# Optimization experiments

Measured on AMD Instinct MI355X. Metric: run time of the kernel, lower is better.

Reference implementation:

```python
import jax, jax.numpy as jnp
import numpy as np

N_HEADS = 8
WINDOW = 4
KS = 3
N_LAYERS = 6
EPS = 1e-5


def _rel_to_abs(x):
    # x: [B,H,L,2L-1] relative logits -> [B,H,L,L] absolute
    b, h, l, _ = x.shape
    x = jnp.pad(x, ((0, 0), (0, 0), (0, 0), (0, 1)))
    x = x.reshape(b, h, l * 2 * l)
    x = jnp.pad(x, ((0, 0), (0, 0), (0, l - 1)))
    return x.reshape(b, h, l + 1, 2 * l - 1)[:, :, :l, l - 1:]


def _abs_to_rel(x):
    # x: [B,H,L,L] -> [B,H,L,2L-1]
    b, h, l, _ = x.shape
    x = jnp.pad(x, ((0, 0), (0, 0), (0, 0), (0, l - 1)))
    x = x.reshape(b, h, l * (2 * l - 1))
    x = jnp.pad(x, ((0, 0), (0, 0), (l, 0)))
    return x.reshape(b, h, l, 2 * l)[:, :, :, 1:]


def _get_rel_emb(emb, t):
    # emb: [2*WINDOW+1, D] -> [2t-1, D]
    pad = max(t - (WINDOW + 1), 0)
    start = max((WINDOW + 1) - t, 0)
    emb = jnp.pad(emb, ((pad, pad), (0, 0)))
    return emb[start:start + 2 * t - 1]


def _layer_norm(x, g, b):
    # normalize over channel dim (axis 1) of [B,C,T]
    m = jnp.mean(x, axis=1, keepdims=True)
    v = jnp.mean((x - m) ** 2, axis=1, keepdims=True)
    return (x - m) * jax.lax.rsqrt(v + EPS) * g[None, :, None] + b[None, :, None]


def _attn(x, w, bvec, erk, erv, attn_mask):
    # x: [B,C,T]; w: [4,C,C] (q,k,v,o 1x1 convs); bvec: [4,C]
    B, C, T = x.shape
    kch = C // N_HEADS

    def proj(i):
        h = jnp.einsum('oc,bct->bot', w[i], x) + bvec[i][None, :, None]
        return h.reshape(B, N_HEADS, kch, T).transpose(0, 1, 3, 2)  # [B,H,T,D]

    q, k, v = proj(0), proj(1), proj(2)
    scale = np.float32(1.0 / np.sqrt(kch))
    scores = jnp.einsum('bhtd,bhsd->bhts', q * scale, k)
    kr = _get_rel_emb(erk, T)  # [2T-1, D]
    scores = scores + _rel_to_abs(jnp.einsum('bhtd,md->bhtm', q * scale, kr))
    scores = jnp.where(attn_mask == 0, jnp.float32(-1e4), scores)
    p = jax.nn.softmax(scores, axis=-1)
    out = jnp.einsum('bhts,bhsd->bhtd', p, v)
    vr = _get_rel_emb(erv, T)
    out = out + jnp.einsum('bhtm,md->bhtd', _abs_to_rel(p), vr)
    out = out.transpose(0, 1, 3, 2).reshape(B, C, T)
    return jnp.einsum('oc,bct->bot', w[3], out) + bvec[3][None, :, None]


def _conv1d_same(h, wt, bt):
    pad_l, pad_r = (KS - 1) // 2, KS // 2
    hp = jnp.pad(h, ((0, 0), (0, 0), (pad_l, pad_r)))
    y = jax.lax.conv_general_dilated(hp, wt, (1,), 'VALID',
                                     dimension_numbers=('NCH', 'OIH', 'NCH'))
    return y + bt[None, :, None]


def _ffn(x, mask, w1, b1, w2, b2):
    h = jax.nn.relu(_conv1d_same(x * mask, w1, b1))  # activation=None -> relu
    return _conv1d_same(h * mask, w2, b2) * mask


def reference(x, x_mask, attn_w, attn_b, erk, erv, ln1_g, ln1_b,
              ffn_w1, ffn_b1, ffn_w2, ffn_b2, ln2_g, ln2_b):
    attn_mask = x_mask[:, :, :, None] * x_mask[:, :, None, :]  # [B,1,T,T]
    x = x * x_mask
    for i in range(N_LAYERS):
        y = _attn(x, attn_w[i], attn_b[i], erk[i], erv[i], attn_mask)
        x = _layer_norm(x + y, ln1_g[i], ln1_b[i])
        y = _ffn(x, x_mask, ffn_w1[i], ffn_b1[i], ffn_w2[i], ffn_b2[i])
        x = _layer_norm(x + y, ln2_g[i], ln2_b[i])
    return x * x_mask


def setup_inputs() -> dict:
    B, C, T, F, L = 8, 512, 1024, 2048, N_LAYERS
    kch = C // N_HEADS
    key = jax.random.key(0)
    ks = jax.random.split(key, 8)
    std = 0.02
    return {
        'x': jax.random.normal(ks[0], (B, C, T), jnp.float32),
        'x_mask': jnp.ones((B, 1, T), jnp.float32),
        'attn_w': jax.random.normal(ks[1], (L, 4, C, C), jnp.float32) * std,
        'attn_b': jnp.zeros((L, 4, C), jnp.float32),
        'erk': jax.random.normal(ks[2], (L, 2 * WINDOW + 1, kch), jnp.float32) * (kch ** -0.5),
        'erv': jax.random.normal(ks[3], (L, 2 * WINDOW + 1, kch), jnp.float32) * (kch ** -0.5),
        'ln1_g': jnp.ones((L, C), jnp.float32),
        'ln1_b': jnp.zeros((L, C), jnp.float32),
        'ffn_w1': jax.random.normal(ks[4], (L, F, C, KS), jnp.float32) * std,
        'ffn_b1': jnp.zeros((L, F), jnp.float32),
        'ffn_w2': jax.random.normal(ks[5], (L, C, F, KS), jnp.float32) * std,
        'ffn_b2': jnp.zeros((L, C), jnp.float32),
        'ln2_g': jnp.ones((L, C), jnp.float32),
        'ln2_b': jnp.zeros((L, C), jnp.float32),
    }
```

## Files before the change

kernel.cpp:

```cpp
#include <hip/hip_runtime.h>

typedef __bf16 bf16_t;
typedef __bf16 bf16x8 __attribute__((ext_vector_type(8)));
typedef __bf16 bf16x4 __attribute__((ext_vector_type(4)));
typedef float  f32x4  __attribute__((ext_vector_type(4)));

#define AS1 __attribute__((address_space(1)))
#define AS3 __attribute__((address_space(3)))

template<int BM, int BN, int OUTMN, int CONV, int BIAS, int RELU, int MASK>
__global__ __launch_bounds__(256)
void gemm_nt(const bf16_t* __restrict__ A, const bf16_t* __restrict__ B,
             bf16_t* __restrict__ C, const float* __restrict__ bias,
             const float* __restrict__ mask, const bf16_t* __restrict__ zpage,
             int K, int lda, int ldb, int ldc, int CIN,
             long sAb, long sAh, long sBb, long sBh, long sCb, long sCh)
{
    constexpr int BK = 32;
    __shared__ bf16_t As[BM * BK];
    __shared__ bf16_t Bs[BN * BK];
    const int z = blockIdx.z;
    int tap0 = 0;
    if constexpr (CONV == 2) {
        tap0 = z;
        A += (long)tap0 * CIN;
    } else {
        A += (long)(z >> 3) * sAb + (long)(z & 7) * sAh;
        B += (long)(z >> 3) * sBb + (long)(z & 7) * sBh;
        C += (long)(z >> 3) * sCb + (long)(z & 7) * sCh;
    }
    const int m0 = blockIdx.y * BM;
    const int n0 = blockIdx.x * BN;
    const int tid = threadIdx.x;
    const int wid = tid >> 6, lane = tid & 63;
    constexpr int WM = BM / 2, WN = BN / 2;
    constexpr int FM = WM / 16, FN = WN / 16;
    const int wm = wid >> 1, wn = wid & 1;

    f32x4 acc[FM][FN] = {};

    constexpr int ACH = BM / 64;
    constexpr int BCH = BN / 64;
    const int rquad = lane >> 2;
    const int koff  = (lane & 3) * 8;

    int tap = 0, cc0 = 0;
    for (int k0 = 0; k0 < K; k0 += BK) {
        #pragma unroll
        for (int q = 0; q < ACH; ++q) {
            int ch  = wid * ACH + q;
            int row = ch * 16 + rquad;
            const bf16_t* src = A + (long)(m0 + row) * lda + (k0 + koff);
            __builtin_amdgcn_global_load_lds((const AS1 void*)src,
                                             (AS3 void*)(As + ch * 512), 16, 0, 0);
        }
        #pragma unroll
        for (int q = 0; q < BCH; ++q) {
            int ch  = wid * BCH + q;
            int row = ch * 16 + rquad;
            const bf16_t* src;
            if constexpr (CONV == 1) {
                int tl = (n0 & 1023) + row + tap - 1;
                src = ((unsigned)tl < 1024u)
                    ? B + (long)(n0 + row + tap - 1) * ldb + (cc0 + koff)
                    : zpage + koff;
            } else if constexpr (CONV == 2) {
                int tl = (n0 & 1023) + row + tap0 - 1;
                src = ((unsigned)tl < 1024u)
                    ? B + (long)(n0 + row + tap0 - 1) * ldb + (k0 + koff)
                    : zpage + koff;
            } else {
                src = B + (long)(n0 + row) * ldb + (k0 + koff);
            }
            __builtin_amdgcn_global_load_lds((const AS1 void*)src,
                                             (AS3 void*)(Bs + ch * 512), 16, 0, 0);
        }
        if constexpr (CONV == 1) { cc0 += BK; if (cc0 == CIN) { cc0 = 0; ++tap; } }
        __syncthreads();

        const bf16_t* Ab = As + (wm * WM + (lane & 15)) * BK + ((lane >> 4) * 8);
        const bf16_t* Bb = Bs + (wn * WN + (lane & 15)) * BK + ((lane >> 4) * 8);
        bf16x8 af[FM], bv[FN];
        #pragma unroll
        for (int i = 0; i < FM; ++i) af[i] = *(const bf16x8*)(Ab + i * 16 * BK);
        #pragma unroll
        for (int j = 0; j < FN; ++j) bv[j] = *(const bf16x8*)(Bb + j * 16 * BK);
        #pragma unroll
        for (int i = 0; i < FM; ++i)
            #pragma unroll
            for (int j = 0; j < FN; ++j)
                acc[i][j] = __builtin_amdgcn_mfma_f32_16x16x32_bf16(af[i], bv[j], acc[i][j], 0, 0, 0);
        __syncthreads();
    }

    const int mw = m0 + wm * WM, nw = n0 + wn * WN;
    #pragma unroll
    for (int i = 0; i < FM; ++i) {
        const int mb = mw + i * 16 + (lane >> 4) * 4;
        f32x4 bvv = {};
        if constexpr (BIAS) bvv = *(const f32x4*)(bias + mb);
        #pragma unroll
        for (int j = 0; j < FN; ++j) {
            const int nn = nw + j * 16 + (lane & 15);
            f32x4 v = acc[i][j];
            if constexpr (BIAS) v += bvv;
            if constexpr (RELU) {
                #pragma unroll
                for (int r = 0; r < 4; ++r) v[r] = fmaxf(v[r], 0.f);
            }
            if constexpr (MASK) v *= mask[nn];
            bf16x4 o;
            #pragma unroll
            for (int r = 0; r < 4; ++r) o[r] = (bf16_t)v[r];
            if constexpr (CONV == 2) {
                *(bf16x4*)(C + ((long)tap0 << 22) + (long)nn * 512 + mb) = o;
            } else if constexpr (OUTMN) {
                #pragma unroll
                for (int r = 0; r < 4; ++r) C[(long)(mb + r) * ldc + nn] = (bf16_t)v[r];
            } else {
                *(bf16x4*)(C + (long)nn * ldc + mb) = o;
            }
        }
    }
}

__global__ __launch_bounds__(256)
void rel_qk(const bf16_t* __restrict__ qk, const float* __restrict__ erk_l,
            float* __restrict__ R)
{
    int gw = blockIdx.x * 4 + (threadIdx.x >> 6);
    int z = gw >> 10, t = gw & 1023;
    int b = z >> 3, h = z & 7;
    int lane = threadIdx.x & 63;
    float qv = (float)qk[(long)(b * 1024 + t) * 1024 + h * 64 + lane];
    float r[9];
    #pragma unroll
    for (int j = 0; j < 9; ++j) r[j] = qv * erk_l[j * 64 + lane];
    #pragma unroll
    for (int o = 1; o < 64; o <<= 1)
        #pragma unroll
        for (int j = 0; j < 9; ++j) r[j] += __shfl_xor(r[j], o);
    if (lane == 0) {
        #pragma unroll
        for (int j = 0; j < 9; ++j) R[(long)gw * 9 + j] = r[j];
    }
}

__global__ __launch_bounds__(256)
void mask_bias(const float* __restrict__ mask, float* __restrict__ kb)
{
    int i = blockIdx.x * 256 + threadIdx.x;
    if (i < 8192) kb[i] = (mask[i] == 0.f) ? -1e4f : 0.f;
}

__global__ __launch_bounds__(256)
void flash_attn(const bf16_t* __restrict__ qk, const bf16_t* __restrict__ vt,
                const float* __restrict__ R, const float* __restrict__ kb,
                bf16_t* __restrict__ out, float* __restrict__ stats)
{
    __shared__ bf16_t P_lds[4 * 1024];
    const int w = threadIdx.x >> 6, lane = threadIdx.x & 63;
    const int hi = lane >> 4, li = lane & 15;
    const int bh = blockIdx.x, b = bh >> 3, h = bh & 7;
    const int q0 = blockIdx.y * 64 + w * 16;
    const long nbase = (long)b * 1024;
    char* pw = (char*)(P_lds + w * 1024);

    const bf16_t* qrow = qk + (nbase + q0 + li) * 1024 + h * 64 + hi * 8;
    bf16x8 aq0 = *(const bf16x8*)(qrow);
    bf16x8 aq1 = *(const bf16x8*)(qrow + 32);

    float m_run[4], l_run[4];
    #pragma unroll
    for (int r = 0; r < 4; ++r) { m_run[r] = -3.0e38f; l_run[r] = 0.f; }
    f32x4 acc_o[4] = {};

    const bf16_t* kbase = qk + nbase * 1024 + 512 + h * 64 + hi * 8;
    const bf16_t* vbase = vt + (long)(h * 64 + li) * 8192 + nbase + hi * 8;
    const float* kbp = kb + b * 1024;

    bf16x8 kc[4][2], vv[4][2];
    #pragma unroll
    for (int j = 0; j < 4; ++j) {
        const bf16_t* kr = kbase + (long)(j * 16 + li) * 1024;
        kc[j][0] = *(const bf16x8*)kr;
        kc[j][1] = *(const bf16x8*)(kr + 32);
    }

    for (int it = 0; it < 16; ++it) {
        const int s0 = it * 64;
        #pragma unroll
        for (int j2 = 0; j2 < 4; ++j2) {
            const bf16_t* vr = vbase + (long)(j2 * 16) * 8192 + s0;
            vv[j2][0] = *(const bf16x8*)vr;
            vv[j2][1] = *(const bf16x8*)(vr + 32);
        }
        float kbv[4];
        #pragma unroll
        for (int j = 0; j < 4; ++j) kbv[j] = kbp[s0 + j * 16 + li];
        f32x4 sc[4];
        __builtin_amdgcn_s_setprio(1);
        #pragma unroll
        for (int j = 0; j < 4; ++j) {
            f32x4 a = {};
            a = __builtin_amdgcn_mfma_f32_16x16x32_bf16(aq0, kc[j][0], a, 0, 0, 0);
            a = __builtin_amdgcn_mfma_f32_16x16x32_bf16(aq1, kc[j][1], a, 0, 0, 0);
            sc[j] = a;
        }
        __builtin_amdgcn_s_setprio(0);
        const int s1 = (s0 + 64) & 1023;
        #pragma unroll
        for (int j = 0; j < 4; ++j) {
            const bf16_t* kr = kbase + (long)(s1 + j * 16 + li) * 1024;
            kc[j][0] = *(const bf16x8*)kr;
            kc[j][1] = *(const bf16x8*)(kr + 32);
        }
        #pragma unroll
        for (int j = 0; j < 4; ++j) {
            const int sb = s0 + j * 16;
            const bool near = (sb + 15 >= q0 - 4) && (sb <= q0 + 19);
            const int s_abs = sb + li;
            #pragma unroll
            for (int r = 0; r < 4; ++r) {
                const int q_abs = q0 + hi * 4 + r;
                float v = sc[j][r] + kbv[j];
                if (near) {
                    int jb = s_abs - q_abs + 4;
                    if ((unsigned)jb < 9u)
                        v += R[((long)bh * 1024 + q_abs) * 9 + jb];
                }
                sc[j][r] = v;
            }
        }
        float tm[4];
        #pragma unroll
        for (int r = 0; r < 4; ++r)
            tm[r] = fmaxf(fmaxf(sc[0][r], sc[1][r]), fmaxf(sc[2][r], sc[3][r]));
        #pragma unroll
        for (int o = 1; o < 16; o <<= 1)
            #pragma unroll
            for (int r = 0; r < 4; ++r) tm[r] = fmaxf(tm[r], __shfl_xor(tm[r], o));
        float scl[4];
        #pragma unroll
        for (int r = 0; r < 4; ++r) {
            float mnew = fmaxf(m_run[r], tm[r]);
            scl[r] = __expf(m_run[r] - mnew);
            m_run[r] = mnew;
        }
        float ls[4] = {0.f, 0.f, 0.f, 0.f};
        #pragma unroll
        for (int j = 0; j < 4; ++j)
            #pragma unroll
            for (int r = 0; r < 4; ++r) {
                float p = __expf(sc[j][r] - m_run[r]);
                sc[j][r] = p;
                ls[r] += p;
            }
        #pragma unroll
        for (int o = 1; o < 16; o <<= 1)
            #pragma unroll
            for (int r = 0; r < 4; ++r) ls[r] += __shfl_xor(ls[r], o);
        #pragma unroll
        for (int r = 0; r < 4; ++r) l_run[r] = l_run[r] * scl[r] + ls[r];
        #pragma unroll
        for (int j2 = 0; j2 < 4; ++j2)
            #pragma unroll
            for (int r = 0; r < 4; ++r) acc_o[j2][r] *= scl[r];
        #pragma unroll
        for (int j = 0; j < 4; ++j)
            #pragma unroll
            for (int r = 0; r < 4; ++r) {
                int q = hi * 4 + r;
                int c = (j * 32 + li * 2) ^ ((q & 7) << 4);
                *(bf16_t*)(pw + q * 128 + c) = (bf16_t)sc[j][r];
            }
        asm volatile("s_waitcnt lgkmcnt(0)" ::: "memory");
        __builtin_amdgcn_s_setprio(1);
        #pragma unroll
        for (int half = 0; half < 2; ++half) {
            int cr = (half * 64 + hi * 16) ^ ((li & 7) << 4);
            bf16x8 pa = *(const bf16x8*)(pw + li * 128 + cr);
            #pragma unroll
            for (int j2 = 0; j2 < 4; ++j2)
                acc_o[j2] = __builtin_amdgcn_mfma_f32_16x16x32_bf16(pa, vv[j2][half], acc_o[j2], 0, 0, 0);
        }
        __builtin_amdgcn_s_setprio(0);
    }

    #pragma unroll
    for (int r = 0; r < 4; ++r) {
        const float inv = 1.f / l_run[r];
        const int q_abs = q0 + hi * 4 + r;
        #pragma unroll
        for (int j2 = 0; j2 < 4; ++j2) {
            const int d = j2 * 16 + li;
            out[(nbase + q_abs) * 512 + h * 64 + d] = (bf16_t)(acc_o[j2][r] * inv);
        }
        if (li == 0) {
            stats[2 * ((long)bh * 1024 + q_abs)]     = m_run[r];
            stats[2 * ((long)bh * 1024 + q_abs) + 1] = l_run[r];
        }
    }
}

__global__ __launch_bounds__(256)
void band_finish(const bf16_t* __restrict__ qk, const float* __restrict__ R,
                 const float* __restrict__ stats, const float* __restrict__ erv_l,
                 const float* __restrict__ kb, bf16_t* __restrict__ out)
{
    int gw = blockIdx.x * 4 + (threadIdx.x >> 6);
    int bh = gw >> 10, t = gw & 1023;
    int b = bh >> 3, h = bh & 7;
    int lane = threadIdx.x & 63;
    const long nb = (long)b * 1024;
    float qv = (float)qk[(nb + t) * 1024 + h * 64 + lane];
    float p[9];
    #pragma unroll
    for (int j = 0; j < 9; ++j) {
        int s = t + j - 4;
        float dot = 0.f;
        if ((unsigned)s < 1024u)
            dot = qv * (float)qk[(nb + s) * 1024 + 512 + h * 64 + lane];
        p[j] = dot;
    }
    #pragma unroll
    for (int o = 1; o < 64; o <<= 1)
        #pragma unroll
        for (int j = 0; j < 9; ++j) p[j] += __shfl_xor(p[j], o);
    float m = stats[2 * (long)gw], invl = 1.f / stats[2 * (long)gw + 1];
    #pragma unroll
    for (int j = 0; j < 9; ++j) {
        int s = t + j - 4;
        if ((unsigned)s < 1024u) {
            float sc = p[j] + R[(long)gw * 9 + j] + kb[b * 1024 + s];
            p[j] = __expf(sc - m) * invl;
        } else p[j] = 0.f;
    }
    long oidx = (nb + t) * 512 + h * 64 + lane;
    float v = (float)out[oidx];
    #pragma unroll
    for (int j = 0; j < 9; ++j) v += p[j] * erv_l[j * 64 + lane];
    out[oidx] = (bf16_t)v;
}

template<int MASKOUT>
__global__ __launch_bounds__(256)
void ln_residual(float* __restrict__ xres, const bf16_t* __restrict__ y,
                 bf16_t* __restrict__ xbf, const float* __restrict__ g,
                 const float* __restrict__ bvec, const float* __restrict__ mask)
{
    int gw = blockIdx.x * 4 + (threadIdx.x >> 6);
    int lane = threadIdx.x & 63;
    long base = (long)gw * 512 + lane * 8;
    f32x4 x0 = *(const f32x4*)(xres + base);
    f32x4 x1 = *(const f32x4*)(xres + base + 4);
    bf16x8 yv = *(const bf16x8*)(y + base);
    float s[8];
    #pragma unroll
    for (int e = 0; e < 4; ++e) { s[e] = x0[e] + (float)yv[e]; s[4 + e] = x1[e] + (float)yv[4 + e]; }
    float sum = 0.f, sq = 0.f;
    #pragma unroll
    for (int e = 0; e < 8; ++e) { sum += s[e]; sq += s[e] * s[e]; }
    #pragma unroll
    for (int o = 1; o < 64; o <<= 1) { sum += __shfl_xor(sum, o); sq += __shfl_xor(sq, o); }
    float mean = sum * (1.f / 512.f);
    float var  = sq * (1.f / 512.f) - mean * mean;
    float rstd = rsqrtf(var + 1e-5f);
    f32x4 g0 = *(const f32x4*)(g + lane * 8);
    f32x4 g1 = *(const f32x4*)(g + lane * 8 + 4);
    f32x4 b0 = *(const f32x4*)(bvec + lane * 8);
    f32x4 b1 = *(const f32x4*)(bvec + lane * 8 + 4);
    float mk = MASKOUT ? mask[gw] : 1.f;
    f32x4 o0, o1; bf16x8 ob;
    #pragma unroll
    for (int e = 0; e < 4; ++e) {
        float v0 = (s[e] - mean) * rstd * g0[e] + b0[e];
        float v1 = (s[4 + e] - mean) * rstd * g1[e] + b1[e];
        o0[e] = v0; o1[e] = v1;
        ob[e] = (bf16_t)(v0 * mk); ob[4 + e] = (bf16_t)(v1 * mk);
    }
    *(f32x4*)(xres + base) = o0;
    *(f32x4*)(xres + base + 4) = o1;
    *(bf16x8*)(xbf + base) = ob;
}

__global__ __launch_bounds__(256)
void ln_residual_p3(float* __restrict__ xres, const bf16_t* __restrict__ part,
                    bf16_t* __restrict__ xbf, const float* __restrict__ g,
                    const float* __restrict__ bvec, const float* __restrict__ bias,
                    const float* __restrict__ mask)
{
    int gw = blockIdx.x * 4 + (threadIdx.x >> 6);
    int lane = threadIdx.x & 63;
    long base = (long)gw * 512 + lane * 8;
    bf16x8 pa = *(const bf16x8*)(part + base);
    bf16x8 pbv = *(const bf16x8*)(part + base + (1l << 22));
    bf16x8 pc = *(const bf16x8*)(part + base + (2l << 22));
    f32x4 x0 = *(const f32x4*)(xres + base);
    f32x4 x1 = *(const f32x4*)(xres + base + 4);
    f32x4 bi0 = *(const f32x4*)(bias + lane * 8);
    f32x4 bi1 = *(const f32x4*)(bias + lane * 8 + 4);
    float mk = mask[gw];
    float s[8];
    #pragma unroll
    for (int e = 0; e < 4; ++e) {
        float y0 = ((float)pa[e] + (float)pbv[e] + (float)pc[e] + bi0[e]) * mk;
        float y1 = ((float)pa[4 + e] + (float)pbv[4 + e] + (float)pc[4 + e] + bi1[e]) * mk;
        s[e] = x0[e] + y0; s[4 + e] = x1[e] + y1;
    }
    float sum = 0.f, sq = 0.f;
    #pragma unroll
    for (int e = 0; e < 8; ++e) { sum += s[e]; sq += s[e] * s[e]; }
    #pragma unroll
    for (int o = 1; o < 64; o <<= 1) { sum += __shfl_xor(sum, o); sq += __shfl_xor(sq, o); }
    float mean = sum * (1.f / 512.f);
    float var  = sq * (1.f / 512.f) - mean * mean;
    float rstd = rsqrtf(var + 1e-5f);
    f32x4 g0 = *(const f32x4*)(g + lane * 8);
    f32x4 g1 = *(const f32x4*)(g + lane * 8 + 4);
    f32x4 b0 = *(const f32x4*)(bvec + lane * 8);
    f32x4 b1 = *(const f32x4*)(bvec + lane * 8 + 4);
    f32x4 o0, o1; bf16x8 ob;
    #pragma unroll
    for (int e = 0; e < 4; ++e) {
        float v0 = (s[e] - mean) * rstd * g0[e] + b0[e];
        float v1 = (s[4 + e] - mean) * rstd * g1[e] + b1[e];
        o0[e] = v0; o1[e] = v1;
        ob[e] = (bf16_t)v0; ob[4 + e] = (bf16_t)v1;
    }
    *(f32x4*)(xres + base) = o0;
    *(f32x4*)(xres + base + 4) = o1;
    *(bf16x8*)(xbf + base) = ob;
}

__global__ __launch_bounds__(256)
void transpose_in_k(const float* __restrict__ x, const float* __restrict__ mask,
                    float* __restrict__ xres, bf16_t* __restrict__ xbf)
{
    __shared__ float tile[32][33];
    int b = blockIdx.z, c0 = blockIdx.y * 32, t0 = blockIdx.x * 32;
    int tx = threadIdx.x & 31, ty = threadIdx.x >> 5;
    #pragma unroll
    for (int r = 0; r < 4; ++r) {
        int cl = ty + r * 8;
        tile[cl][tx] = x[((long)b * 512 + c0 + cl) * 1024 + t0 + tx];
    }
    __syncthreads();
    #pragma unroll
    for (int r = 0; r < 4; ++r) {
        int tl = ty + r * 8;
        int n = b * 1024 + t0 + tl;
        float v = tile[tx][tl] * mask[n];
        xres[(long)n * 512 + c0 + tx] = v;
        xbf[(long)n * 512 + c0 + tx] = (bf16_t)v;
    }
}

__global__ __launch_bounds__(256)
void transpose_out_k(const float* __restrict__ xres, const float* __restrict__ mask,
                     float* __restrict__ out)
{
    __shared__ float tile[32][33];
    int b = blockIdx.z, c0 = blockIdx.y * 32, t0 = blockIdx.x * 32;
    int tx = threadIdx.x & 31, ty = threadIdx.x >> 5;
    #pragma unroll
    for (int r = 0; r < 4; ++r) {
        int tl = ty + r * 8;
        int n = b * 1024 + t0 + tl;
        tile[tl][tx] = xres[(long)n * 512 + c0 + tx] * mask[n];
    }
    __syncthreads();
    #pragma unroll
    for (int r = 0; r < 4; ++r) {
        int cl = ty + r * 8;
        out[((long)b * 512 + c0 + cl) * 1024 + t0 + tx] = tile[tx][cl];
    }
}

__global__ __launch_bounds__(256)
void pack_attn_w(const float* __restrict__ w, bf16_t* __restrict__ Wqk,
                 bf16_t* __restrict__ Wv, bf16_t* __restrict__ Wo)
{
    int idx = blockIdx.x * 256 + threadIdx.x;
    if (idx >= 4 * 512 * 512) return;
    int c = idx & 511;
    int o = (idx >> 9) & 511;
    int which = idx >> 18;
    float v = w[idx];
    if (which == 0) v *= 0.125f;
    if (which <= 1)      Wqk[(which * 512 + o) * 512 + c] = (bf16_t)v;
    else if (which == 2) Wv[o * 512 + c] = (bf16_t)v;
    else                 Wo[o * 512 + c] = (bf16_t)v;
}

__global__ __launch_bounds__(256)
void pack_attn_b(const float* __restrict__ bsrc, float* __restrict__ bqk)
{
    int idx = blockIdx.x * 256 + threadIdx.x;
    if (idx >= 6 * 2 * 512) return;
    int c = idx & 511, which = (idx >> 9) & 1, i = idx >> 10;
    float v = bsrc[(i * 4 + which) * 512 + c];
    if (which == 0) v *= 0.125f;
    bqk[i * 1024 + which * 512 + c] = v;
}

__global__ __launch_bounds__(256)
void pack_w1k(const float* __restrict__ w, bf16_t* __restrict__ Wp)
{
    int idx = blockIdx.x * 256 + threadIdx.x;
    if (idx >= 2048 * 1536) return;
    int c = idx & 511;
    int k = (idx >> 9) % 3;
    int f = idx / 1536;
    Wp[idx] = (bf16_t)w[(f * 512 + c) * 3 + k];
}

__global__ __launch_bounds__(256)
void pack_w2k(const float* __restrict__ w, bf16_t* __restrict__ Wp)
{
    int idx = blockIdx.x * 256 + threadIdx.x;
    if (idx >= 512 * 6144) return;
    int f = idx & 2047;
    int k = (idx >> 11) % 3;
    int ci = idx / 6144;
    Wp[idx] = (bf16_t)w[ci * 6144 + f * 3 + k];
}

extern "C" void kernel_launch(void* const* d_in, const int* in_sizes, int n_in,
                              void* d_out, int out_size, void* d_ws, size_t ws_size,
                              hipStream_t stream)
{
    const float* x      = (const float*)d_in[0];
    const float* xmask  = (const float*)d_in[1];
    const float* attn_w = (const float*)d_in[2];
    const float* attn_b = (const float*)d_in[3];
    const float* erk    = (const float*)d_in[4];
    const float* erv    = (const float*)d_in[5];
    const float* ln1g   = (const float*)d_in[6];
    const float* ln1b   = (const float*)d_in[7];
    const float* w1     = (const float*)d_in[8];
    const float* b1in   = (const float*)d_in[9];
    const float* w2     = (const float*)d_in[10];
    const float* b2in   = (const float*)d_in[11];
    const float* ln2g   = (const float*)d_in[12];
    const float* ln2b   = (const float*)d_in[13];
    float* out = (float*)d_out;

    char* p = (char*)d_ws;
    auto alloc = [&](size_t bytes) {
        char* r = p;
        p += (bytes + 255) & ~(size_t)255;
        return r;
    };
    bf16_t* zpage = (bf16_t*)alloc(1024);
    bf16_t* Wqk_l = (bf16_t*)alloc(1024l * 512 * 2);
    bf16_t* Wv_l  = (bf16_t*)alloc(512l * 512 * 2);
    bf16_t* Wo_l  = (bf16_t*)alloc(512l * 512 * 2);
    bf16_t* W1p_l = (bf16_t*)alloc(2048l * 1536 * 2);
    bf16_t* W2p_l = (bf16_t*)alloc(512l * 6144 * 2);
    float*  bqk   = (float*)alloc(6l * 1024 * 4);
    float*  xres  = (float*)alloc(8192l * 512 * 4);
    bf16_t* xbf   = (bf16_t*)alloc(8192l * 512 * 2);
    bf16_t* big   = (bf16_t*)alloc(8192l * 2048 * 2);
    bf16_t* ybuf  = (bf16_t*)alloc(8192l * 512 * 2);
    bf16_t* part  = (bf16_t*)alloc(3l * 8192 * 512 * 2);
    float*  R     = (float*)alloc(64l * 1024 * 9 * 4);
    float*  stats = (float*)alloc(64l * 1024 * 2 * 4);
    float*  kb    = (float*)alloc(8192l * 4);
    (void)in_sizes; (void)n_in; (void)out_size; (void)ws_size;

    bf16_t* qk       = big;
    bf16_t* vt       = big + 8192l * 1024;
    bf16_t* attn_out = vt + 512l * 8192;
    bf16_t* hbuf     = big;

    hipMemsetAsync(zpage, 0, 1024, stream);
    pack_attn_b<<<24, 256, 0, stream>>>(attn_b, bqk);
    mask_bias<<<32, 256, 0, stream>>>(xmask, kb);
    transpose_in_k<<<dim3(32, 16, 8), 256, 0, stream>>>(x, xmask, xres, xbf);

    for (int i = 0; i < 6; ++i) {
        pack_attn_w<<<4096, 256, 0, stream>>>(attn_w + (long)i * 4 * 512 * 512,
                                              Wqk_l, Wv_l, Wo_l);
        pack_w1k<<<12288, 256, 0, stream>>>(w1 + (long)i * 2048 * 512 * 3, W1p_l);
        pack_w2k<<<12288, 256, 0, stream>>>(w2 + (long)i * 512 * 2048 * 3, W2p_l);

        gemm_nt<128, 128, 0, 0, 1, 0, 0><<<dim3(64, 8, 1), 256, 0, stream>>>(
            Wqk_l, xbf, qk, bqk + i * 1024, nullptr, zpage,
            512, 512, 512, 1024, 0, 0, 0, 0, 0, 0, 0);
        gemm_nt<64, 128, 1, 0, 1, 0, 0><<<dim3(64, 8, 1), 256, 0, stream>>>(
            Wv_l, xbf, vt, attn_b + (i * 4 + 2) * 512, nullptr, zpage,
            512, 512, 512, 8192, 0, 0, 0, 0, 0, 0, 0);
        rel_qk<<<16384, 256, 0, stream>>>(qk, erk + i * 576, R);
        flash_attn<<<dim3(64, 16), 256, 0, stream>>>(qk, vt, R, kb,
                                                     attn_out, stats);
        band_finish<<<16384, 256, 0, stream>>>(qk, R, stats, erv + i * 576,
                                               kb, attn_out);
        gemm_nt<64, 128, 0, 0, 1, 0, 0><<<dim3(64, 8, 1), 256, 0, stream>>>(
            Wo_l, attn_out, ybuf, attn_b + (i * 4 + 3) * 512, nullptr, zpage,
            512, 512, 512, 512, 0, 0, 0, 0, 0, 0, 0);
        ln_residual<1><<<2048, 256, 0, stream>>>(xres, ybuf, xbf,
                                                 ln1g + i * 512, ln1b + i * 512, xmask);
        gemm_nt<128, 128, 0, 1, 1, 1, 1><<<dim3(64, 16, 1), 256, 0, stream>>>(
            W1p_l, xbf, hbuf, b1in + i * 2048, xmask, zpage,
            1536, 1536, 512, 2048, 512, 0, 0, 0, 0, 0, 0);
        gemm_nt<64, 128, 0, 2, 0, 0, 0><<<dim3(64, 8, 3), 256, 0, stream>>>(
            W2p_l, hbuf, part, nullptr, nullptr, zpage,
            2048, 6144, 2048, 512, 2048, 0, 0, 0, 0, 0, 0);
        ln_residual_p3<<<2048, 256, 0, stream>>>(xres, part, xbf,
                                                 ln2g + i * 512, ln2b + i * 512,
                                                 b2in + i * 512, xmask);
    }

    transpose_out_k<<<dim3(32, 16, 8), 256, 0, stream>>>(xres, xmask, out);
}
```

Before: 2.897 ms.

## Split attention key range across two blocks and merge partials in finish kernel

Flash attention now launches twice as many blocks, each covering half of the key sequence, and writes unnormalized partial outputs plus per-split max/sum statistics. The band finishing kernel becomes a combine step that rescales and merges the two partials before adding the relative-value term. This targets low occupancy of the attention kernel. In exchange it adds a second partial output buffer, extra memory traffic, and stores unnormalized partials in bf16, which may cost some accuracy.

```diff
diff --git a/kernel.cpp b/kernel.cpp
--- a/kernel.cpp
+++ b/kernel.cpp
@@ -156,12 +156,15 @@
 __global__ __launch_bounds__(256)
 void flash_attn(const bf16_t* __restrict__ qk, const bf16_t* __restrict__ vt,
                 const float* __restrict__ R, const float* __restrict__ kb,
-                bf16_t* __restrict__ out, float* __restrict__ stats)
+                bf16_t* __restrict__ o0, bf16_t* __restrict__ o1,
+                float* __restrict__ stats)
 {
     __shared__ bf16_t P_lds[4 * 1024];
     const int w = threadIdx.x >> 6, lane = threadIdx.x & 63;
     const int hi = lane >> 4, li = lane & 15;
     const int bh = blockIdx.x, b = bh >> 3, h = bh & 7;
+    const int sh = blockIdx.z;
+    const int sbeg = sh * 512;
     const int q0 = blockIdx.y * 64 + w * 16;
     const long nbase = (long)b * 1024;
     char* pw = (char*)(P_lds + w * 1024);
@@ -182,13 +185,13 @@
     bf16x8 kc[4][2], vv[4][2];
     #pragma unroll
     for (int j = 0; j < 4; ++j) {
-        const bf16_t* kr = kbase + (long)(j * 16 + li) * 1024;
+        const bf16_t* kr = kbase + (long)(sbeg + j * 16 + li) * 1024;
         kc[j][0] = *(const bf16x8*)kr;
         kc[j][1] = *(const bf16x8*)(kr + 32);
     }
 
-    for (int it = 0; it < 16; ++it) {
-        const int s0 = it * 64;
+    for (int it = 0; it < 8; ++it) {
+        const int s0 = sbeg + it * 64;
         #pragma unroll
         for (int j2 = 0; j2 < 4; ++j2) {
             const bf16_t* vr = vbase + (long)(j2 * 16) * 8192 + s0;
@@ -208,7 +211,7 @@
             sc[j] = a;
         }
         __builtin_amdgcn_s_setprio(0);
-        const int s1 = (s0 + 64) & 1023;
+        const int s1 = sbeg + ((it + 1) & 7) * 64;
         #pragma unroll
         for (int j = 0; j < 4; ++j) {
             const bf16_t* kr = kbase + (long)(s1 + j * 16 + li) * 1024;
@@ -287,26 +290,28 @@
         __builtin_amdgcn_s_setprio(0);
     }
 
+    bf16_t* op = sh ? o1 : o0;
+    const long sstat = (long)sh * 65536;
     #pragma unroll
     for (int r = 0; r < 4; ++r) {
-        const float inv = 1.f / l_run[r];
         const int q_abs = q0 + hi * 4 + r;
         #pragma unroll
         for (int j2 = 0; j2 < 4; ++j2) {
             const int d = j2 * 16 + li;
-            out[(nbase + q_abs) * 512 + h * 64 + d] = (bf16_t)(acc_o[j2][r] * inv);
+            op[(nbase + q_abs) * 512 + h * 64 + d] = (bf16_t)acc_o[j2][r];
         }
         if (li == 0) {
-            stats[2 * ((long)bh * 1024 + q_abs)]     = m_run[r];
-            stats[2 * ((long)bh * 1024 + q_abs) + 1] = l_run[r];
-        }
-    }
-}
-
-__global__ __launch_bounds__(256)
-void band_finish(const bf16_t* __restrict__ qk, const float* __restrict__ R,
-                 const float* __restrict__ stats, const float* __restrict__ erv_l,
-                 const float* __restrict__ kb, bf16_t* __restrict__ out)
+            stats[2 * (sstat + (long)bh * 1024 + q_abs)]     = m_run[r];
+            stats[2 * (sstat + (long)bh * 1024 + q_abs) + 1] = l_run[r];
+        }
+    }
+}
+
+__global__ __launch_bounds__(256)
+void combine_finish(const bf16_t* __restrict__ qk, const float* __restrict__ R,
+                    const float* __restrict__ stats, const float* __restrict__ erv_l,
+                    const float* __restrict__ kb, const bf16_t* __restrict__ o1,
+                    bf16_t* __restrict__ out)
 {
     int gw = blockIdx.x * 4 + (threadIdx.x >> 6);
     int bh = gw >> 10, t = gw & 1023;
@@ -327,7 +332,11 @@
     for (int o = 1; o < 64; o <<= 1)
         #pragma unroll
         for (int j = 0; j < 9; ++j) p[j] += __shfl_xor(p[j], o);
-    float m = stats[2 * (long)gw], invl = 1.f / stats[2 * (long)gw + 1];
+    float m1 = stats[2 * (long)gw],           l1 = stats[2 * (long)gw + 1];
+    float m2 = stats[2 * (65536l + gw)],      l2 = stats[2 * (65536l + gw) + 1];
+    float m  = fmaxf(m1, m2);
+    float w1 = __expf(m1 - m), w2 = __expf(m2 - m);
+    float invl = 1.f / (w1 * l1 + w2 * l2);
     #pragma unroll
     for (int j = 0; j < 9; ++j) {
         int s = t + j - 4;
@@ -337,7 +346,7 @@
         } else p[j] = 0.f;
     }
     long oidx = (nb + t) * 512 + h * 64 + lane;
-    float v = (float)out[oidx];
+    float v = (w1 * (float)out[oidx] + w2 * (float)o1[oidx]) * invl;
     #pragma unroll
     for (int j = 0; j < 9; ++j) v += p[j] * erv_l[j * 64 + lane];
     out[oidx] = (bf16_t)v;
@@ -564,8 +573,9 @@
     bf16_t* big   = (bf16_t*)alloc(8192l * 2048 * 2);
     bf16_t* ybuf  = (bf16_t*)alloc(8192l * 512 * 2);
     bf16_t* part  = (bf16_t*)alloc(3l * 8192 * 512 * 2);
+    bf16_t* opart = (bf16_t*)alloc(8192l * 512 * 2);
     float*  R     = (float*)alloc(64l * 1024 * 9 * 4);
-    float*  stats = (float*)alloc(64l * 1024 * 2 * 4);
+    float*  stats = (float*)alloc(2l * 64 * 1024 * 2 * 4);
     float*  kb    = (float*)alloc(8192l * 4);
     (void)in_sizes; (void)n_in; (void)out_size; (void)ws_size;
 
@@ -592,10 +602,10 @@
             Wv_l, xbf, vt, attn_b + (i * 4 + 2) * 512, nullptr, zpage,
             512, 512, 512, 8192, 0, 0, 0, 0, 0, 0, 0);
         rel_qk<<<16384, 256, 0, stream>>>(qk, erk + i * 576, R);
-        flash_attn<<<dim3(64, 16), 256, 0, stream>>>(qk, vt, R, kb,
-                                                     attn_out, stats);
-        band_finish<<<16384, 256, 0, stream>>>(qk, R, stats, erv + i * 576,
-                                               kb, attn_out);
+        flash_attn<<<dim3(64, 16, 2), 256, 0, stream>>>(qk, vt, R, kb,
+                                                        attn_out, opart, stats);
+        combine_finish<<<16384, 256, 0, stream>>>(qk, R, stats, erv + i * 576,
+                                                  kb, opart, attn_out);
         gemm_nt<64, 128, 0, 0, 1, 0, 0><<<dim3(64, 8, 1), 256, 0, stream>>>(
             Wo_l, attn_out, ybuf, attn_b + (i * 4 + 3) * 512, nullptr, zpage,
             512, 512, 512, 512, 0, 0, 0, 0, 0, 0, 0);
```

Result: no change. 2.944 ms (+1.6%).
